# Kernel tuning notes

Measured on AMD Instinct MI355X. Metric: run time of the kernel, lower is better.

The kernel has to match this reference:

```python
import jax, jax.numpy as jnp
import numpy as np
from jax import lax

D_MODEL, D_INNER, D_STATE, DT_RANK, D_CONV = 512, 1024, 16, 32, 4
B, L = 4, 1024

def setup_inputs() -> dict:
    key = jax.random.key(0)
    ks = jax.random.split(key, 10)
    s = lambda k, shp, sc=0.02: jax.random.normal(k, shp, jnp.float32) * sc
    x = jax.random.normal(ks[0], (B, L, D_MODEL), jnp.float32)
    in_proj_w = s(ks[1], (2 * D_INNER, D_MODEL))
    conv_w = s(ks[2], (D_INNER, 1, D_CONV), 0.1)
    conv_b = jnp.zeros((D_INNER,), jnp.float32)
    x_proj_w = s(ks[3], (DT_RANK + 2 * D_STATE, D_INNER))
    dt_proj_w = s(ks[4], (D_INNER, DT_RANK), DT_RANK ** -0.5)
    dt_proj_b = s(ks[5], (D_INNER,), 0.1)
    # S4D-real init: A_log = log(1..d_state) per channel
    A_log = jnp.log(jnp.tile(jnp.arange(1, D_STATE + 1, dtype=jnp.float32), (D_INNER, 1)))
    D = jnp.ones((D_INNER,), jnp.float32)
    out_proj_w = s(ks[6], (D_MODEL, D_INNER))
    return dict(x=x, in_proj_w=in_proj_w, conv_w=conv_w, conv_b=conv_b,
                x_proj_w=x_proj_w, dt_proj_w=dt_proj_w, dt_proj_b=dt_proj_b,
                A_log=A_log, D=D, out_proj_w=out_proj_w)

def _mamba_fwd(x, in_proj_w, conv_w, conv_b, x_proj_w, dt_proj_w, dt_proj_b, A_log, D, out_proj_w):
    # in_proj and split into ssm branch / gate branch
    xz = jnp.einsum('bld,ed->ble', x, in_proj_w)          # [B,L,2*d_inner]
    xc, z = jnp.split(xz, 2, axis=-1)
    # depthwise causal conv1d along L (torch pads d_conv-1 both sides then slices [:L])
    xt = jnp.transpose(xc, (0, 2, 1))                      # [B,d_inner,L]
    xt = lax.conv_general_dilated(xt, conv_w, (1,), [(D_CONV - 1, 0)],
                                  feature_group_count=D_INNER,
                                  dimension_numbers=('NCH', 'OIH', 'NCH'))
    xc = jnp.transpose(xt + conv_b[None, :, None], (0, 2, 1))  # [B,L,d_inner]
    xc = jax.nn.silu(xc)
    # input-dependent SSM params
    dbc = jnp.einsum('bld,ed->ble', xc, x_proj_w)          # [B,L,dt_rank+2*d_state]
    dt, Bm, Cm = jnp.split(dbc, [DT_RANK, DT_RANK + D_STATE], axis=-1)
    delta = jax.nn.softplus(jnp.einsum('blr,dr->bld', dt, dt_proj_w) + dt_proj_b)  # [B,L,d_inner]
    A = -jnp.exp(A_log)                                    # [d_inner,d_state]
    deltaA = jnp.exp(delta[..., None] * A)                 # [B,L,d_inner,d_state]
    deltaBx = delta[..., None] * Bm[:, :, None, :] * xc[..., None]
    # parallel (associative) scan: h_t = deltaA_t * h_{t-1} + deltaBx_t
    def combine(c1, c2):
        a1, b1 = c1
        a2, b2 = c2
        return a2 * a1, a2 * b1 + b2
    _, h = lax.associative_scan(combine, (deltaA, deltaBx), axis=1)
    y = jnp.sum(h * Cm[:, :, None, :], axis=-1) + D * xc   # [B,L,d_inner]
    y = y * jax.nn.silu(z)
    return jnp.einsum('bld,ed->ble', y, out_proj_w)        # [B,L,d_model]

def reference(x, in_proj_w, conv_w, conv_b, x_proj_w, dt_proj_w, dt_proj_b, A_log, D, out_proj_w):
    return _mamba_fwd(x, in_proj_w, conv_w, conv_b, x_proj_w, dt_proj_w, dt_proj_b, A_log, D, out_proj_w)
```

## Files before the change

### kernel.cpp

```cpp
#include <hip/hip_runtime.h>
#include <cstddef>
#include <cstdint>

#define DMODEL 512
#define DINNER 1024
#define DSTATE 16
#define DTRANK 32
#define DCONV  4
#define NB     4
#define NL     1024
#define NR     (NB * NL)
#define CH     32
#define NCHUNK (NL / CH)
#define LOG2E  1.4426950408889634f
#define LN2    0.6931471805599453f

typedef __attribute__((ext_vector_type(8))) short bf16x8;
typedef __attribute__((ext_vector_type(4))) float f32x4;

__device__ __forceinline__ unsigned short f2bf(float f) {
    unsigned u = __builtin_bit_cast(unsigned, f);
    unsigned r = u + 0x7FFFu + ((u >> 16) & 1u);
    return (unsigned short)(r >> 16);
}

__device__ __forceinline__ void gload_lds16(const unsigned short* g, unsigned short* lds) {
    __builtin_amdgcn_global_load_lds(
        (const __attribute__((address_space(1))) void*)g,
        (__attribute__((address_space(3))) void*)lds, 16, 0, 0);
}

__global__ __launch_bounds__(256) void cast_all_kernel(
    const float* __restrict__ x, const float* __restrict__ w_in,
    const float* __restrict__ w_out, const float* __restrict__ w_xp,
    unsigned short* __restrict__ xh, unsigned short* __restrict__ wih,
    unsigned short* __restrict__ woh, unsigned short* __restrict__ xpwh)
{
    int i = blockIdx.x * 256 + threadIdx.x;
    const float* src; unsigned short* dst;
    if (i < 524288)       { src = x;     dst = xh;   }
    else if (i < 786432)  { src = w_in;  dst = wih;  i -= 524288; }
    else if (i < 917504)  { src = w_out; dst = woh;  i -= 786432; }
    else if (i < 933888)  { src = w_xp;  dst = xpwh; i -= 917504; }
    else return;
    float4 v = ((const float4*)src)[i];
    ushort4 o;
    o.x = f2bf(v.x); o.y = f2bf(v.y); o.z = f2bf(v.z); o.w = f2bf(v.w);
    ((ushort4*)dst)[i] = o;
}

template<int BN>
__global__ __launch_bounds__(256) void gemm_bf16_kernel(
    const unsigned short* __restrict__ A, const unsigned short* __restrict__ Bw,
    float* __restrict__ C, int M, int N, int K)
{
    constexpr int BK = 64;
    constexpr int NFRAG = BN / 32;
    constexpr int BINSTR = BN / 32;
    __shared__ unsigned short As[128 * BK];
    __shared__ unsigned short Bs[BN * BK];

    const int tid  = threadIdx.x;
    const int lane = tid & 63;
    const int w    = tid >> 6;
    const int wm   = w >> 1, wn = w & 1;
    const int brow = blockIdx.y * 128;
    const int bcol = blockIdx.x * BN;

    const int srcslot = (lane & 7) ^ (lane >> 3);
    const unsigned short* ag[4];
    unsigned short* al[4];
#pragma unroll
    for (int i = 0; i < 4; ++i) {
        const int r = w * 32 + i * 8 + (lane >> 3);
        ag[i] = A + (size_t)(brow + r) * K + srcslot * 8;
        al[i] = As + (w * 256 + i * 64) * 8;
    }
    const unsigned short* bg[BINSTR];
    unsigned short* bl[BINSTR];
#pragma unroll
    for (int i = 0; i < BINSTR; ++i) {
        const int r = w * 8 * BINSTR + i * 8 + (lane >> 3);
        bg[i] = Bw + (size_t)(bcol + r) * K + srcslot * 8;
        bl[i] = Bs + (w * 64 * BINSTR + i * 64) * 8;
    }

    const int fr = lane & 15;
    const int fq = lane >> 4;
    f32x4 acc[4][NFRAG] = {};

    for (int k0 = 0; k0 < K; k0 += BK) {
#pragma unroll
        for (int i = 0; i < 4; ++i) gload_lds16(ag[i] + k0, al[i]);
#pragma unroll
        for (int i = 0; i < BINSTR; ++i) gload_lds16(bg[i] + k0, bl[i]);
        __syncthreads();
#pragma unroll
        for (int ks = 0; ks < 2; ++ks) {
            bf16x8 af[4], bfr[NFRAG];
#pragma unroll
            for (int m = 0; m < 4; ++m) {
                const int r = wm * 64 + m * 16 + fr;
                const int s = (ks * 4 + fq) ^ (r & 7);
                af[m] = *(const bf16x8*)(As + r * BK + s * 8);
            }
#pragma unroll
            for (int n = 0; n < NFRAG; ++n) {
                const int r = wn * (BN / 2) + n * 16 + fr;
                const int s = (ks * 4 + fq) ^ (r & 7);
                bfr[n] = *(const bf16x8*)(Bs + r * BK + s * 8);
            }
#pragma unroll
            for (int m = 0; m < 4; ++m)
#pragma unroll
                for (int n = 0; n < NFRAG; ++n)
                    acc[m][n] = __builtin_amdgcn_mfma_f32_16x16x32_bf16(
                        af[m], bfr[n], acc[m][n], 0, 0, 0);
        }
        __syncthreads();
    }

    const int row0 = brow + wm * 64;
    const int col0 = bcol + wn * (BN / 2);
#pragma unroll
    for (int m = 0; m < 4; ++m)
#pragma unroll
        for (int n = 0; n < NFRAG; ++n)
#pragma unroll
            for (int j = 0; j < 4; ++j)
                C[(size_t)(row0 + m * 16 + fq * 4 + j) * N + col0 + n * 16 + fr] = acc[m][n][j];
}

__global__ __launch_bounds__(256) void conv_silu_kernel(
    const float* __restrict__ xz, const float* __restrict__ conv_w,
    const float* __restrict__ conv_b, float* __restrict__ xc,
    unsigned short* __restrict__ xch)
{
    const int idx4 = blockIdx.x * 256 + threadIdx.x;
    const int e4 = idx4 & (DINNER / 4 - 1);
    const int r  = idx4 >> 8;
    const int l  = r & (NL - 1);
    const float4 cb = ((const float4*)conv_b)[e4];
    float4 w[4];
#pragma unroll
    for (int c = 0; c < 4; ++c) w[c] = ((const float4*)conv_w)[e4 * 4 + c];
    const float4 zero = {0.f, 0.f, 0.f, 0.f};
    const float4 v0 = (l >= 3) ? ((const float4*)(xz + (size_t)(r - 3) * 2 * DINNER))[e4] : zero;
    const float4 v1 = (l >= 2) ? ((const float4*)(xz + (size_t)(r - 2) * 2 * DINNER))[e4] : zero;
    const float4 v2 = (l >= 1) ? ((const float4*)(xz + (size_t)(r - 1) * 2 * DINNER))[e4] : zero;
    const float4 v3 = ((const float4*)(xz + (size_t)r * 2 * DINNER))[e4];
    float4 o;
    o.x = cb.x + w[0].x * v0.x + w[0].y * v1.x + w[0].z * v2.x + w[0].w * v3.x;
    o.y = cb.y + w[1].x * v0.y + w[1].y * v1.y + w[1].z * v2.y + w[1].w * v3.y;
    o.z = cb.z + w[2].x * v0.z + w[2].y * v1.z + w[2].z * v2.z + w[2].w * v3.z;
    o.w = cb.w + w[3].x * v0.w + w[3].y * v1.w + w[3].z * v2.w + w[3].w * v3.w;
    float4 s;
    s.x = o.x * __builtin_amdgcn_rcpf(1.f + __builtin_amdgcn_exp2f(-o.x * LOG2E));
    s.y = o.y * __builtin_amdgcn_rcpf(1.f + __builtin_amdgcn_exp2f(-o.y * LOG2E));
    s.z = o.z * __builtin_amdgcn_rcpf(1.f + __builtin_amdgcn_exp2f(-o.z * LOG2E));
    s.w = o.w * __builtin_amdgcn_rcpf(1.f + __builtin_amdgcn_exp2f(-o.w * LOG2E));
    ((float4*)xc)[idx4] = s;
    ushort4 h4;
    h4.x = f2bf(s.x); h4.y = f2bf(s.y); h4.z = f2bf(s.z); h4.w = f2bf(s.w);
    ((ushort4*)xch)[idx4] = h4;
}

#define DRT 32
__global__ __launch_bounds__(256) void delta_kernel(
    const float* __restrict__ dbc, const float* __restrict__ dtw,
    const float* __restrict__ dtb, float* __restrict__ delta)
{
    __shared__ float dlds[DRT * DTRANK];
    const int t = threadIdx.x;
    const int e = blockIdx.x * 256 + t;
    const int r0 = blockIdx.y * DRT;
    for (int i = t; i < DRT * DTRANK; i += 256) {
        const int row = i >> 5, jj = i & 31;
        dlds[i] = dbc[(size_t)(r0 + row) * 64 + jj];
    }
    float4 wv[8];
    const float4* dtw4 = (const float4*)(dtw + (size_t)e * DTRANK);
#pragma unroll
    for (int q = 0; q < 8; ++q) wv[q] = dtw4[q];
    const float bias = dtb[e];
    __syncthreads();
#pragma unroll 4
    for (int row = 0; row < DRT; ++row) {
        const float4* dl4 = (const float4*)(dlds + row * DTRANK);
        float sum = bias;
#pragma unroll
        for (int q = 0; q < 8; ++q) {
            const float4 dv = dl4[q];
            const float4 w = wv[q];
            sum += dv.x * w.x + dv.y * w.y + dv.z * w.z + dv.w * w.w;
        }
        const float u = __builtin_amdgcn_exp2f(-fabsf(sum) * LOG2E);
        delta[(size_t)(r0 + row) * DINNER + e] =
            fmaxf(sum, 0.f) + __builtin_amdgcn_logf(1.f + u) * LN2;
    }
}

__global__ __launch_bounds__(256) void scanA_kernel(
    const float* __restrict__ delta, const float* __restrict__ xc,
    const float* __restrict__ dbc, const float* __restrict__ A_log,
    float* __restrict__ chunkP, float* __restrict__ chunkS)
{
    const int tid = threadIdx.x;
    const int e = blockIdx.x * 256 + tid;
    const int b = blockIdx.y, ck = blockIdx.z;
    const int rbase = b * NL + ck * CH;

    float dlv[CH], xvv[CH];
    const float* dp = delta + (size_t)rbase * DINNER + e;
    const float* xp = xc + (size_t)rbase * DINNER + e;
#pragma unroll
    for (int l = 0; l < CH; ++l) {
        dlv[l] = dp[(size_t)l * DINNER];
        xvv[l] = xp[(size_t)l * DINNER];
    }

    float Aes2[DSTATE];
    const float4* al4 = (const float4*)(A_log + (size_t)e * DSTATE);
#pragma unroll
    for (int q = 0; q < 4; ++q) {
        const float4 a = al4[q];
        Aes2[q * 4 + 0] = -__expf(a.x) * LOG2E;
        Aes2[q * 4 + 1] = -__expf(a.y) * LOG2E;
        Aes2[q * 4 + 2] = -__expf(a.z) * LOG2E;
        Aes2[q * 4 + 3] = -__expf(a.w) * LOG2E;
    }

    float S[DSTATE];
#pragma unroll
    for (int s = 0; s < DSTATE; ++s) S[s] = 0.f;
    float cum = 0.f;
#pragma unroll
    for (int l = 0; l < CH; ++l) {
        const float* bu = dbc + (size_t)(rbase + l) * 64 + DTRANK;
        cum += dlv[l];
        const float common = dlv[l] * xvv[l];
#pragma unroll
        for (int s = 0; s < DSTATE; ++s) {
            const float dA = __builtin_amdgcn_exp2f(dlv[l] * Aes2[s]);
            S[s] = fmaf(dA, S[s], common * bu[s]);
        }
    }
    const size_t oi = (((size_t)b * NCHUNK + ck) * DINNER + e) * DSTATE;
    float4* Pp = (float4*)(chunkP + oi);
    float4* Sp = (float4*)(chunkS + oi);
#pragma unroll
    for (int q = 0; q < 4; ++q) {
        float4 pv, sv;
        pv.x = __builtin_amdgcn_exp2f(cum * Aes2[q * 4 + 0]);
        pv.y = __builtin_amdgcn_exp2f(cum * Aes2[q * 4 + 1]);
        pv.z = __builtin_amdgcn_exp2f(cum * Aes2[q * 4 + 2]);
        pv.w = __builtin_amdgcn_exp2f(cum * Aes2[q * 4 + 3]);
        sv.x = S[q * 4 + 0]; sv.y = S[q * 4 + 1];
        sv.z = S[q * 4 + 2]; sv.w = S[q * 4 + 3];
        Pp[q] = pv; Sp[q] = sv;
    }
}

__global__ __launch_bounds__(256) void scanB_kernel(
    const float* __restrict__ chunkP, float* __restrict__ chunkS)
{
    const int idx = blockIdx.x * 256 + threadIdx.x;
    const int b = idx >> 14;
    const int rem = idx & (DINNER * DSTATE - 1);
    const size_t base = (size_t)b * NCHUNK * (DINNER * DSTATE) + rem;
    float P[NCHUNK], S[NCHUNK];
#pragma unroll
    for (int c = 0; c < NCHUNK; ++c) {
        P[c] = chunkP[base + (size_t)c * (DINNER * DSTATE)];
        S[c] = chunkS[base + (size_t)c * (DINNER * DSTATE)];
    }
    float h = 0.f;
#pragma unroll
    for (int c = 0; c < NCHUNK; ++c) {
        chunkS[base + (size_t)c * (DINNER * DSTATE)] = h;
        h = fmaf(P[c], h, S[c]);
    }
}

__global__ __launch_bounds__(256) void scanC_kernel(
    const float* __restrict__ xz, const float* __restrict__ xc,
    const float* __restrict__ dbc, const float* __restrict__ A_log,
    const float* __restrict__ Dp, const float* __restrict__ hinit,
    const float* __restrict__ delta, unsigned short* __restrict__ yh)
{
    const int tid = threadIdx.x;
    const int e = blockIdx.x * 256 + tid;
    const int b = blockIdx.y, ck = blockIdx.z;
    const int rbase = b * NL + ck * CH;

    float dlv[CH], xvv[CH], zvv[CH];
    const float* dp = delta + (size_t)rbase * DINNER + e;
    const float* xp = xc + (size_t)rbase * DINNER + e;
    const float* zp = xz + (size_t)rbase * (2 * DINNER) + DINNER + e;
#pragma unroll
    for (int l = 0; l < CH; ++l) {
        dlv[l] = dp[(size_t)l * DINNER];
        xvv[l] = xp[(size_t)l * DINNER];
        zvv[l] = zp[(size_t)l * 2 * DINNER];
    }

    float Aes2[DSTATE];
    const float4* al4 = (const float4*)(A_log + (size_t)e * DSTATE);
#pragma unroll
    for (int q = 0; q < 4; ++q) {
        const float4 a = al4[q];
        Aes2[q * 4 + 0] = -__expf(a.x) * LOG2E;
        Aes2[q * 4 + 1] = -__expf(a.y) * LOG2E;
        Aes2[q * 4 + 2] = -__expf(a.z) * LOG2E;
        Aes2[q * 4 + 3] = -__expf(a.w) * LOG2E;
    }

    float h[DSTATE];
    const size_t oi = (((size_t)b * NCHUNK + ck) * DINNER + e) * DSTATE;
    const float4* h4 = (const float4*)(hinit + oi);
#pragma unroll
    for (int q = 0; q < 4; ++q) {
        const float4 v = h4[q];
        h[q * 4 + 0] = v.x; h[q * 4 + 1] = v.y; h[q * 4 + 2] = v.z; h[q * 4 + 3] = v.w;
    }
    const float Dv = Dp[e];
    unsigned short* yp = yh + (size_t)rbase * DINNER + e;

#pragma unroll
    for (int l = 0; l < CH; ++l) {
        const float* bu = dbc + (size_t)(rbase + l) * 64 + DTRANK;
        const float common = dlv[l] * xvv[l];
        float y = 0.f;
#pragma unroll
        for (int s = 0; s < DSTATE; ++s) {
            const float dA = __builtin_amdgcn_exp2f(dlv[l] * Aes2[s]);
            h[s] = fmaf(dA, h[s], common * bu[s]);
            y = fmaf(h[s], bu[DSTATE + s], y);
        }
        y = fmaf(Dv, xvv[l], y);
        const float zv = zvv[l];
        const float sig = __builtin_amdgcn_rcpf(1.f + __builtin_amdgcn_exp2f(-zv * LOG2E));
        yp[(size_t)l * DINNER] = f2bf(y * (zv * sig));
    }
}

extern "C" void kernel_launch(void* const* d_in, const int* in_sizes, int n_in,
                              void* d_out, int out_size, void* d_ws, size_t ws_size,
                              hipStream_t stream)
{
    const float* x          = (const float*)d_in[0];
    const float* in_proj_w  = (const float*)d_in[1];
    const float* conv_w     = (const float*)d_in[2];
    const float* conv_b     = (const float*)d_in[3];
    const float* x_proj_w   = (const float*)d_in[4];
    const float* dt_proj_w  = (const float*)d_in[5];
    const float* dt_proj_b  = (const float*)d_in[6];
    const float* A_log      = (const float*)d_in[7];
    const float* Dp         = (const float*)d_in[8];
    const float* out_proj_w = (const float*)d_in[9];
    float* out = (float*)d_out;

    float* ws  = (float*)d_ws;
    float* xz     = ws;
    float* xc     = xz + (size_t)NR * 2 * DINNER;
    float* dbc    = xc + (size_t)NR * DINNER;
    float* yb     = dbc + (size_t)NR * 64;
    float* chunkS = yb + (size_t)NR * DINNER;
    float* chunkP = chunkS + (size_t)NB * NCHUNK * DINNER * DSTATE;
    unsigned short* xch = (unsigned short*)(chunkP + (size_t)NB * NCHUNK * DINNER * DSTATE);
    unsigned short* yh  = xch;
    unsigned short* xh  = xch;
    unsigned short* wih = xch + (size_t)NR * DINNER;
    unsigned short* woh = wih + (size_t)2 * DINNER * DMODEL;
    unsigned short* xpwh = woh + (size_t)DMODEL * DINNER;

    cast_all_kernel<<<(933888 + 255) / 256, 256, 0, stream>>>(
        x, in_proj_w, out_proj_w, x_proj_w, xh, wih, woh, xpwh);

    gemm_bf16_kernel<128><<<dim3(2 * DINNER / 128, NR / 128), 256, 0, stream>>>(
        xh, wih, xz, NR, 2 * DINNER, DMODEL);
    conv_silu_kernel<<<NR * DINNER / 1024, 256, 0, stream>>>(xz, conv_w, conv_b, xc, xch);
    gemm_bf16_kernel<64><<<dim3(1, NR / 128), 256, 0, stream>>>(
        xch, xpwh, dbc, NR, 64, DINNER);
    delta_kernel<<<dim3(DINNER / 256, NR / DRT), 256, 0, stream>>>(
        dbc, dt_proj_w, dt_proj_b, yb);
    scanA_kernel<<<dim3(DINNER / 256, NB, NCHUNK), 256, 0, stream>>>(
        yb, xc, dbc, A_log, chunkP, chunkS);
    scanB_kernel<<<NB * DINNER * DSTATE / 256, 256, 0, stream>>>(chunkP, chunkS);
    scanC_kernel<<<dim3(DINNER / 256, NB, NCHUNK), 256, 0, stream>>>(
        xz, xc, dbc, A_log, Dp, chunkS, yb, yh);
    gemm_bf16_kernel<64><<<dim3(DMODEL / 64, NR / 128), 256, 0, stream>>>(
        yh, woh, out, NR, DMODEL, DINNER);
}
```

Before: 153.3 us.

## Store in_proj output and conv activations in bf16 to cut memory traffic

The in_proj GEMM now writes xz in bf16 rather than fp32. The conv kernel reads that bf16 buffer and writes only the bf16 copy of xc, dropping the fp32 xc store. The scan kernels read x and z from these bf16 buffers, and their per-chunk register preload arrays are replaced by loads inside a loop that is no longer fully unrolled. This roughly halves the traffic on the largest intermediates, at the cost of lower precision for z and for x as used in the scan, plus possible load-latency exposure from the streaming loads.

```diff
diff --git a/kernel.cpp b/kernel.cpp
--- a/kernel.cpp
+++ b/kernel.cpp
@@ -23,6 +23,9 @@
     unsigned r = u + 0x7FFFu + ((u >> 16) & 1u);
     return (unsigned short)(r >> 16);
 }
+__device__ __forceinline__ float bf2f(unsigned short h) {
+    return __builtin_bit_cast(float, (unsigned)h << 16);
+}
 
 __device__ __forceinline__ void gload_lds16(const unsigned short* g, unsigned short* lds) {
     __builtin_amdgcn_global_load_lds(
@@ -49,10 +52,10 @@
     ((ushort4*)dst)[i] = o;
 }
 
-template<int BN>
+template<int BN, int OUTBF>
 __global__ __launch_bounds__(256) void gemm_bf16_kernel(
     const unsigned short* __restrict__ A, const unsigned short* __restrict__ Bw,
-    float* __restrict__ C, int M, int N, int K)
+    void* __restrict__ Cv, int M, int N, int K)
 {
     constexpr int BK = 64;
     constexpr int NFRAG = BN / 32;
@@ -127,14 +130,16 @@
 #pragma unroll
         for (int n = 0; n < NFRAG; ++n)
 #pragma unroll
-            for (int j = 0; j < 4; ++j)
-                C[(size_t)(row0 + m * 16 + fq * 4 + j) * N + col0 + n * 16 + fr] = acc[m][n][j];
+            for (int j = 0; j < 4; ++j) {
+                const size_t ci = (size_t)(row0 + m * 16 + fq * 4 + j) * N + col0 + n * 16 + fr;
+                if (OUTBF) ((unsigned short*)Cv)[ci] = f2bf(acc[m][n][j]);
+                else       ((float*)Cv)[ci] = acc[m][n][j];
+            }
 }
 
 __global__ __launch_bounds__(256) void conv_silu_kernel(
-    const float* __restrict__ xz, const float* __restrict__ conv_w,
-    const float* __restrict__ conv_b, float* __restrict__ xc,
-    unsigned short* __restrict__ xch)
+    const unsigned short* __restrict__ xzh, const float* __restrict__ conv_w,
+    const float* __restrict__ conv_b, unsigned short* __restrict__ xch)
 {
     const int idx4 = blockIdx.x * 256 + threadIdx.x;
     const int e4 = idx4 & (DINNER / 4 - 1);
@@ -144,22 +149,21 @@
     float4 w[4];
 #pragma unroll
     for (int c = 0; c < 4; ++c) w[c] = ((const float4*)conv_w)[e4 * 4 + c];
-    const float4 zero = {0.f, 0.f, 0.f, 0.f};
-    const float4 v0 = (l >= 3) ? ((const float4*)(xz + (size_t)(r - 3) * 2 * DINNER))[e4] : zero;
-    const float4 v1 = (l >= 2) ? ((const float4*)(xz + (size_t)(r - 2) * 2 * DINNER))[e4] : zero;
-    const float4 v2 = (l >= 1) ? ((const float4*)(xz + (size_t)(r - 1) * 2 * DINNER))[e4] : zero;
-    const float4 v3 = ((const float4*)(xz + (size_t)r * 2 * DINNER))[e4];
+    const ushort4 uz = {0, 0, 0, 0};
+    const ushort4 u0 = (l >= 3) ? ((const ushort4*)(xzh + (size_t)(r - 3) * 2 * DINNER))[e4] : uz;
+    const ushort4 u1 = (l >= 2) ? ((const ushort4*)(xzh + (size_t)(r - 2) * 2 * DINNER))[e4] : uz;
+    const ushort4 u2 = (l >= 1) ? ((const ushort4*)(xzh + (size_t)(r - 1) * 2 * DINNER))[e4] : uz;
+    const ushort4 u3 = ((const ushort4*)(xzh + (size_t)r * 2 * DINNER))[e4];
     float4 o;
-    o.x = cb.x + w[0].x * v0.x + w[0].y * v1.x + w[0].z * v2.x + w[0].w * v3.x;
-    o.y = cb.y + w[1].x * v0.y + w[1].y * v1.y + w[1].z * v2.y + w[1].w * v3.y;
-    o.z = cb.z + w[2].x * v0.z + w[2].y * v1.z + w[2].z * v2.z + w[2].w * v3.z;
-    o.w = cb.w + w[3].x * v0.w + w[3].y * v1.w + w[3].z * v2.w + w[3].w * v3.w;
+    o.x = cb.x + w[0].x * bf2f(u0.x) + w[0].y * bf2f(u1.x) + w[0].z * bf2f(u2.x) + w[0].w * bf2f(u3.x);
+    o.y = cb.y + w[1].x * bf2f(u0.y) + w[1].y * bf2f(u1.y) + w[1].z * bf2f(u2.y) + w[1].w * bf2f(u3.y);
+    o.z = cb.z + w[2].x * bf2f(u0.z) + w[2].y * bf2f(u1.z) + w[2].z * bf2f(u2.z) + w[2].w * bf2f(u3.z);
+    o.w = cb.w + w[3].x * bf2f(u0.w) + w[3].y * bf2f(u1.w) + w[3].z * bf2f(u2.w) + w[3].w * bf2f(u3.w);
     float4 s;
     s.x = o.x * __builtin_amdgcn_rcpf(1.f + __builtin_amdgcn_exp2f(-o.x * LOG2E));
     s.y = o.y * __builtin_amdgcn_rcpf(1.f + __builtin_amdgcn_exp2f(-o.y * LOG2E));
     s.z = o.z * __builtin_amdgcn_rcpf(1.f + __builtin_amdgcn_exp2f(-o.z * LOG2E));
     s.w = o.w * __builtin_amdgcn_rcpf(1.f + __builtin_amdgcn_exp2f(-o.w * LOG2E));
-    ((float4*)xc)[idx4] = s;
     ushort4 h4;
     h4.x = f2bf(s.x); h4.y = f2bf(s.y); h4.z = f2bf(s.z); h4.w = f2bf(s.w);
     ((ushort4*)xch)[idx4] = h4;
@@ -201,7 +205,7 @@
 }
 
 __global__ __launch_bounds__(256) void scanA_kernel(
-    const float* __restrict__ delta, const float* __restrict__ xc,
+    const float* __restrict__ delta, const unsigned short* __restrict__ xch,
     const float* __restrict__ dbc, const float* __restrict__ A_log,
     float* __restrict__ chunkP, float* __restrict__ chunkS)
 {
@@ -209,15 +213,6 @@
     const int e = blockIdx.x * 256 + tid;
     const int b = blockIdx.y, ck = blockIdx.z;
     const int rbase = b * NL + ck * CH;
-
-    float dlv[CH], xvv[CH];
-    const float* dp = delta + (size_t)rbase * DINNER + e;
-    const float* xp = xc + (size_t)rbase * DINNER + e;
-#pragma unroll
-    for (int l = 0; l < CH; ++l) {
-        dlv[l] = dp[(size_t)l * DINNER];
-        xvv[l] = xp[(size_t)l * DINNER];
-    }
 
     float Aes2[DSTATE];
     const float4* al4 = (const float4*)(A_log + (size_t)e * DSTATE);
@@ -234,14 +229,17 @@
 #pragma unroll
     for (int s = 0; s < DSTATE; ++s) S[s] = 0.f;
     float cum = 0.f;
-#pragma unroll
+    const float* dp = delta + (size_t)rbase * DINNER + e;
+    const unsigned short* xp = xch + (size_t)rbase * DINNER + e;
     for (int l = 0; l < CH; ++l) {
+        const float dl = dp[(size_t)l * DINNER];
+        const float xv = bf2f(xp[(size_t)l * DINNER]);
         const float* bu = dbc + (size_t)(rbase + l) * 64 + DTRANK;
-        cum += dlv[l];
-        const float common = dlv[l] * xvv[l];
+        cum += dl;
+        const float common = dl * xv;
 #pragma unroll
         for (int s = 0; s < DSTATE; ++s) {
-            const float dA = __builtin_amdgcn_exp2f(dlv[l] * Aes2[s]);
+            const float dA = __builtin_amdgcn_exp2f(dl * Aes2[s]);
             S[s] = fmaf(dA, S[s], common * bu[s]);
         }
     }
@@ -283,7 +281,7 @@
 }
 
 __global__ __launch_bounds__(256) void scanC_kernel(
-    const float* __restrict__ xz, const float* __restrict__ xc,
+    const unsigned short* __restrict__ xzh, const unsigned short* __restrict__ xch,
     const float* __restrict__ dbc, const float* __restrict__ A_log,
     const float* __restrict__ Dp, const float* __restrict__ hinit,
     const float* __restrict__ delta, unsigned short* __restrict__ yh)
@@ -292,17 +290,6 @@
     const int e = blockIdx.x * 256 + tid;
     const int b = blockIdx.y, ck = blockIdx.z;
     const int rbase = b * NL + ck * CH;
-
-    float dlv[CH], xvv[CH], zvv[CH];
-    const float* dp = delta + (size_t)rbase * DINNER + e;
-    const float* xp = xc + (size_t)rbase * DINNER + e;
-    const float* zp = xz + (size_t)rbase * (2 * DINNER) + DINNER + e;
-#pragma unroll
-    for (int l = 0; l < CH; ++l) {
-        dlv[l] = dp[(size_t)l * DINNER];
-        xvv[l] = xp[(size_t)l * DINNER];
-        zvv[l] = zp[(size_t)l * 2 * DINNER];
-    }
 
     float Aes2[DSTATE];
     const float4* al4 = (const float4*)(A_log + (size_t)e * DSTATE);
@@ -324,21 +311,26 @@
         h[q * 4 + 0] = v.x; h[q * 4 + 1] = v.y; h[q * 4 + 2] = v.z; h[q * 4 + 3] = v.w;
     }
     const float Dv = Dp[e];
+
+    const float* dp = delta + (size_t)rbase * DINNER + e;
+    const unsigned short* xp = xch + (size_t)rbase * DINNER + e;
+    const unsigned short* zp = xzh + (size_t)rbase * (2 * DINNER) + DINNER + e;
     unsigned short* yp = yh + (size_t)rbase * DINNER + e;
 
-#pragma unroll
     for (int l = 0; l < CH; ++l) {
+        const float dl = dp[(size_t)l * DINNER];
+        const float xv = bf2f(xp[(size_t)l * DINNER]);
+        const float zv = bf2f(zp[(size_t)l * 2 * DINNER]);
         const float* bu = dbc + (size_t)(rbase + l) * 64 + DTRANK;
-        const float common = dlv[l] * xvv[l];
+        const float common = dl * xv;
         float y = 0.f;
 #pragma unroll
         for (int s = 0; s < DSTATE; ++s) {
-            const float dA = __builtin_amdgcn_exp2f(dlv[l] * Aes2[s]);
+            const float dA = __builtin_amdgcn_exp2f(dl * Aes2[s]);
             h[s] = fmaf(dA, h[s], common * bu[s]);
             y = fmaf(h[s], bu[DSTATE + s], y);
         }
-        y = fmaf(Dv, xvv[l], y);
-        const float zv = zvv[l];
+        y = fmaf(Dv, xv, y);
         const float sig = __builtin_amdgcn_rcpf(1.f + __builtin_amdgcn_exp2f(-zv * LOG2E));
         yp[(size_t)l * DINNER] = f2bf(y * (zv * sig));
     }
@@ -360,35 +352,34 @@
     const float* out_proj_w = (const float*)d_in[9];
     float* out = (float*)d_out;
 
-    float* ws  = (float*)d_ws;
-    float* xz     = ws;
-    float* xc     = xz + (size_t)NR * 2 * DINNER;
-    float* dbc    = xc + (size_t)NR * DINNER;
+    float* ws     = (float*)d_ws;
+    float* dbc    = ws;
     float* yb     = dbc + (size_t)NR * 64;
     float* chunkS = yb + (size_t)NR * DINNER;
     float* chunkP = chunkS + (size_t)NB * NCHUNK * DINNER * DSTATE;
-    unsigned short* xch = (unsigned short*)(chunkP + (size_t)NB * NCHUNK * DINNER * DSTATE);
-    unsigned short* yh  = xch;
-    unsigned short* xh  = xch;
-    unsigned short* wih = xch + (size_t)NR * DINNER;
-    unsigned short* woh = wih + (size_t)2 * DINNER * DMODEL;
+    unsigned short* xzh  = (unsigned short*)(chunkP + (size_t)NB * NCHUNK * DINNER * DSTATE);
+    unsigned short* xch  = xzh + (size_t)NR * 2 * DINNER;
+    unsigned short* yh   = xch + (size_t)NR * DINNER;
+    unsigned short* xh   = yh + (size_t)NR * DINNER;
+    unsigned short* wih  = xh + (size_t)NR * DMODEL;
+    unsigned short* woh  = wih + (size_t)2 * DINNER * DMODEL;
     unsigned short* xpwh = woh + (size_t)DMODEL * DINNER;
 
     cast_all_kernel<<<(933888 + 255) / 256, 256, 0, stream>>>(
         x, in_proj_w, out_proj_w, x_proj_w, xh, wih, woh, xpwh);
 
-    gemm_bf16_kernel<128><<<dim3(2 * DINNER / 128, NR / 128), 256, 0, stream>>>(
-        xh, wih, xz, NR, 2 * DINNER, DMODEL);
-    conv_silu_kernel<<<NR * DINNER / 1024, 256, 0, stream>>>(xz, conv_w, conv_b, xc, xch);
-    gemm_bf16_kernel<64><<<dim3(1, NR / 128), 256, 0, stream>>>(
+    gemm_bf16_kernel<128, 1><<<dim3(2 * DINNER / 128, NR / 128), 256, 0, stream>>>(
+        xh, wih, xzh, NR, 2 * DINNER, DMODEL);
+    conv_silu_kernel<<<NR * DINNER / 1024, 256, 0, stream>>>(xzh, conv_w, conv_b, xch);
+    gemm_bf16_kernel<64, 0><<<dim3(1, NR / 128), 256, 0, stream>>>(
         xch, xpwh, dbc, NR, 64, DINNER);
     delta_kernel<<<dim3(DINNER / 256, NR / DRT), 256, 0, stream>>>(
         dbc, dt_proj_w, dt_proj_b, yb);
     scanA_kernel<<<dim3(DINNER / 256, NB, NCHUNK), 256, 0, stream>>>(
-        yb, xc, dbc, A_log, chunkP, chunkS);
+        yb, xch, dbc, A_log, chunkP, chunkS);
     scanB_kernel<<<NB * DINNER * DSTATE / 256, 256, 0, stream>>>(chunkP, chunkS);
     scanC_kernel<<<dim3(DINNER / 256, NB, NCHUNK), 256, 0, stream>>>(
-        xz, xc, dbc, A_log, Dp, chunkS, yb, yh);
-    gemm_bf16_kernel<64><<<dim3(DMODEL / 64, NR / 128), 256, 0, stream>>>(
+        xzh, xch, dbc, A_log, Dp, chunkS, yb, yh);
+    gemm_bf16_kernel<64, 0><<<dim3(DMODEL / 64, NR / 128), 256, 0, stream>>>(
         yh, woh, out, NR, DMODEL, DINNER);
 }
```

Measured after the change: 133.7 us. -12.8%, faster.
